# Optimization experiments

Measured on AMD Instinct MI355X. Metric: run time of the kernel, lower is better.

## Reference

```python
import jax, jax.numpy as jnp
import numpy as np

D = 128          # hidden_dim
R = 16           # num_relations
N = 50000        # num_nodes
E = 800000       # num_edges
P = 256          # number of candidate paths
L = 4            # path length in nodes (max_path_length=3 edges)
NUM_LAYERS = 2


def _layer_norm(x, g, b, eps=1e-5):
    mu = jnp.mean(x, axis=-1, keepdims=True)
    var = jnp.var(x, axis=-1, keepdims=True)
    return (x - mu) * jax.lax.rsqrt(var + eps) * g + b


def _lstm(x, W_ih, W_hh, b):
    # x: (P, L, 2D) -> final hidden state (P, D). PyTorch gate order i,f,g,o.
    h0 = jnp.zeros((x.shape[0], D), x.dtype)
    c0 = jnp.zeros((x.shape[0], D), x.dtype)
    xs = jnp.swapaxes(x, 0, 1)  # (L, P, 2D)

    def step(carry, xt):
        h, c = carry
        gates = xt @ W_ih.T + h @ W_hh.T + b
        i, f, g, o = jnp.split(gates, 4, axis=-1)
        c = jax.nn.sigmoid(f) * c + jax.nn.sigmoid(i) * jnp.tanh(g)
        h = jax.nn.sigmoid(o) * jnp.tanh(c)
        return (h, c), None

    (h, _), _ = jax.lax.scan(step, (h0, c0), xs)
    return h


def setup_inputs() -> dict:
    key = jax.random.key(0)
    ks = jax.random.split(key, 24)
    s = 0.02
    inp = {
        'node_features': jax.random.normal(ks[0], (N, D), jnp.float32),
        'edge_index': jax.random.randint(ks[1], (2, E), 0, N),
        'edge_types': jax.random.randint(ks[2], (E,), 0, R),
        'query_embedding': jax.random.normal(ks[3], (D,), jnp.float32),
        'path_nodes': jax.random.randint(ks[4], (P, L), 0, N),
        'path_relations': jax.random.randint(ks[5], (P, L - 1), 0, R),
        # RGCN params (stacked over layers)
        'W_self': jax.random.normal(ks[6], (NUM_LAYERS, D, D), jnp.float32) * s,
        'b_self': jnp.zeros((NUM_LAYERS, D), jnp.float32),
        'W_rel': jax.random.normal(ks[7], (NUM_LAYERS, R, D, D), jnp.float32) * s,
        'ln_g': jnp.ones((NUM_LAYERS, D), jnp.float32),
        'ln_b': jnp.zeros((NUM_LAYERS, D), jnp.float32),
        # PathEncoder
        'rel_emb': jax.random.normal(ks[8], (R, D), jnp.float32) * s,
        'W_ih_f': jax.random.normal(ks[9], (4 * D, 2 * D), jnp.float32) * s,
        'W_hh_f': jax.random.normal(ks[10], (4 * D, D), jnp.float32) * s,
        'b_f': jnp.zeros((4 * D,), jnp.float32),
        'W_ih_b': jax.random.normal(ks[11], (4 * D, 2 * D), jnp.float32) * s,
        'W_hh_b': jax.random.normal(ks[12], (4 * D, D), jnp.float32) * s,
        'b_b': jnp.zeros((4 * D,), jnp.float32),
        'W_op': jax.random.normal(ks[13], (D, 2 * D), jnp.float32) * s,
        'b_op': jnp.zeros((D,), jnp.float32),
        # similarity scorer
        'W_s1': jax.random.normal(ks[14], (D, 2 * D), jnp.float32) * s,
        'b_s1': jnp.zeros((D,), jnp.float32),
        'W_s2': jax.random.normal(ks[15], (1, D), jnp.float32) * s,
        'b_s2': jnp.zeros((1,), jnp.float32),
    }
    return inp


def reference(node_features, edge_index, edge_types, query_embedding,
              path_nodes, path_relations,
              W_self, b_self, W_rel, ln_g, ln_b,
              rel_emb, W_ih_f, W_hh_f, b_f, W_ih_b, W_hh_b, b_b, W_op, b_op,
              W_s1, b_s1, W_s2, b_s2):
    src, dst = edge_index[0], edge_index[1]
    n = node_features.shape[0]
    deg = jnp.zeros((n,), node_features.dtype).at[dst].add(1.0)
    denom = jnp.maximum(deg, 1.0)[:, None]

    # ---- encode_subgraph: RGCN layers + LayerNorm ----
    x = node_features
    for l in range(NUM_LAYERS):
        trans = jnp.einsum('nd,rdk->rnk', x, W_rel[l])       # (R, N, D)
        msg = trans[edge_types, src]                          # (E, D) gather
        agg = jax.ops.segment_sum(msg, dst, num_segments=n) / denom
        x = jax.nn.relu(x @ W_self[l] + b_self[l] + agg)
        x = _layer_norm(x, ln_g[l], ln_b[l])
    encoded = x

    # ---- PathEncoder, batched over P paths ----
    pn = encoded[path_nodes]                                  # (P, L, D)
    rf = rel_emb[path_relations]                              # (P, L-1, D)
    zero_rel = jnp.zeros((rf.shape[0], 1, D), rf.dtype)
    rf = jnp.concatenate([zero_rel, rf], axis=1)              # (P, L, D)
    seq = jnp.concatenate([pn, rf], axis=-1)                  # (P, L, 2D)

    h_f = _lstm(seq, W_ih_f, W_hh_f, b_f)                     # forward final h
    h_b = _lstm(seq[:, ::-1, :], W_ih_b, W_hh_b, b_b)         # backward final h
    pe = jnp.concatenate([h_f, h_b], axis=-1)                 # (P, 2D)
    pe = jax.nn.relu(pe @ W_op.T + b_op)                      # (P, D)

    # ---- similarity scorer ----
    q = jnp.broadcast_to(query_embedding[None, :], pe.shape)
    comb = jnp.concatenate([pe, q], axis=-1)                  # (P, 2D)
    hdn = jax.nn.relu(comb @ W_s1.T + b_s1)
    sim = jax.nn.sigmoid(hdn @ W_s2.T + b_s2).squeeze(-1)     # (P,)

    return encoded, pe, sim
```

## Files before the change

kernel.cpp:

```cpp
#include <hip/hip_runtime.h>


#define NN 50000
#define EE 800000
#define DD 128
#define RR 16
#define PP 256
#define PADN 50048
#define NSLOT 17
#define CSTRIDE 136

typedef __attribute__((ext_vector_type(4))) float f32x4;
typedef __attribute__((ext_vector_type(2))) float f32x2;
typedef __attribute__((ext_vector_type(8))) short s16x8;

__device__ __forceinline__ float bf2f(unsigned int u16v){
    unsigned int u = u16v << 16;
    return __builtin_bit_cast(float, u);
}
__device__ __forceinline__ unsigned short f2bf(float f){
    unsigned int u = __builtin_bit_cast(unsigned int, f);
    u = u + 0x7fffu + ((u >> 16) & 1u);
    return (unsigned short)(u >> 16);
}

__global__ void k_hist(const int* __restrict__ dst, int* __restrict__ deg,
                       int* __restrict__ rank){
    int e = blockIdx.x*256 + threadIdx.x;
    if (e < EE) rank[e] = atomicAdd(&deg[dst[e]], 1);
}
__global__ void k_scan1(const int* __restrict__ deg, int* __restrict__ bsum){
    __shared__ int sm[256];
    int t = threadIdx.x, i = blockIdx.x*256 + t;
    sm[t] = (i < NN) ? deg[i] : 0;
    __syncthreads();
    for (int o = 128; o > 0; o >>= 1){
        if (t < o) sm[t] += sm[t+o];
        __syncthreads();
    }
    if (t == 0) bsum[blockIdx.x] = sm[0];
}
__global__ void k_scan2(const int* __restrict__ bsum, int* __restrict__ boff){
    __shared__ int sm[256];
    int t = threadIdx.x;
    int v = (t < 196) ? bsum[t] : 0;
    sm[t] = v;
    __syncthreads();
    for (int o = 1; o < 256; o <<= 1){
        int x = (t >= o) ? sm[t-o] : 0;
        __syncthreads();
        sm[t] += x;
        __syncthreads();
    }
    boff[t] = sm[t] - v;
}
__global__ void k_scan3(const int* __restrict__ deg, const int* __restrict__ boff,
                        int* __restrict__ row_start){
    __shared__ int sm[256];
    int t = threadIdx.x, i = blockIdx.x*256 + t;
    int v = (i < NN) ? deg[i] : 0;
    sm[t] = v;
    __syncthreads();
    for (int o = 1; o < 256; o <<= 1){
        int x = (t >= o) ? sm[t-o] : 0;
        __syncthreads();
        sm[t] += x;
        __syncthreads();
    }
    if (i < NN) row_start[i] = boff[blockIdx.x] + sm[t] - v;
    if (i == 0) row_start[NN] = EE;
}

#define NB_FILL 3125
#define NB_CVT  25024
#define NB_PREP 3968
__global__ void k_fused(const int* __restrict__ src, const int* __restrict__ dst,
                        const int* __restrict__ et, const int* __restrict__ row_start,
                        const int* __restrict__ rank, unsigned int* __restrict__ csr,
                        const float* __restrict__ nf, unsigned short* __restrict__ xb,
                        const float* __restrict__ W_rel, const float* __restrict__ W_self,
                        const float* __restrict__ Wihf, const float* __restrict__ Wihb,
                        const float* __restrict__ Whhf, const float* __restrict__ Whhb,
                        const float* __restrict__ Wop,  const float* __restrict__ Ws1,
                        unsigned short* __restrict__ Bcat,
                        float* __restrict__ Wiht, float* __restrict__ Whht,
                        float* __restrict__ Wopt, float* __restrict__ Ws1t){
    int b = blockIdx.x;
    if (b < NB_FILL){
        int e = b*256 + threadIdx.x;
        int pos = row_start[dst[e]] + rank[e];
        csr[pos] = ((unsigned int)et[e] << 16) | (unsigned int)src[e];
        return;
    }
    if (b < NB_FILL + NB_CVT){
        int i = (b - NB_FILL)*256 + threadIdx.x;
        int r  = i >> 7;
        int dd = i & 127;
        int d  = (((dd >> 3) ^ (r & 15)) << 3) | (dd & 7);
        xb[i] = (r < NN) ? f2bf(nf[(size_t)r*DD + d]) : (unsigned short)0;
        return;
    }
    int i = (b - NB_FILL - NB_CVT)*256 + threadIdx.x;
    if (i < 557056){
        int l  = i / (NSLOT*DD*DD);
        int r  = i % (NSLOT*DD*DD);
        int s  = r / (DD*DD);
        int r2 = r % (DD*DD);
        int ko = r2 / DD;
        int dd = r2 % DD;
        int d  = (((dd >> 3) ^ (ko & 15)) << 3) | (dd & 7);
        float v = (s < RR) ? W_rel[(((size_t)(l*RR + s))*DD + d)*DD + ko]
                           : W_self[((size_t)l*DD + d)*DD + ko];
        Bcat[i] = f2bf(v);
        return;
    }
    int i2 = i - 557056;
    if (i2 < 131072){ int j=i2/512, g=i2%512; Wiht[i2] = Wihf[g*256+j]; }
    else if (i2 < 262144){ int i3=i2-131072; int j=i3/512, g=i3%512; Wiht[131072+i3] = Wihb[g*256+j]; }
    else if (i2 < 327680){ int i3=i2-262144; int j=i3/512, g=i3%512; Whht[i3] = Whhf[g*128+j]; }
    else if (i2 < 393216){ int i3=i2-327680; int j=i3/512, g=i3%512; Whht[65536+i3] = Whhb[g*128+j]; }
    else if (i2 < 425984){ int i3=i2-393216; int j=i3/128, k=i3%128; Wopt[i3] = Wop[k*256+j]; }
    else if (i2 < 458752){ int i3=i2-425984; int j=i3/128, k=i3%128; Ws1t[i3] = Ws1[k*256+j]; }
}

__global__ __launch_bounds__(256, 2) void k_gemm(const unsigned short* __restrict__ A,
                                                 const unsigned short* __restrict__ Bt,
                                                 unsigned short* __restrict__ C)
{
    __shared__ unsigned short S[32768];
    unsigned short* As = S;
    unsigned short* Bs = S + 16384;
    const int m0 = blockIdx.x * 128;
    const int s  = blockIdx.y;
    const int tid  = threadIdx.x;
    const int wave = tid >> 6;
    const int lane = tid & 63;

    const unsigned short* gA = A + ((size_t)m0 + wave*32)*DD + lane*8;
    const unsigned short* gB = Bt + ((size_t)s*DD + wave*32)*DD + lane*8;
    unsigned short* lA = As + (wave*32)*DD;
    unsigned short* lB = Bs + (wave*32)*DD;
    for (int i = 0; i < 8; ++i){
        __builtin_amdgcn_global_load_lds((__attribute__((address_space(1))) const void*)(gA + i*512),
                                         (__attribute__((address_space(3))) void*)(lA + i*512), 16, 0, 0);
        __builtin_amdgcn_global_load_lds((__attribute__((address_space(1))) const void*)(gB + i*512),
                                         (__attribute__((address_space(3))) void*)(lB + i*512), 16, 0, 0);
    }
    __syncthreads();

    const int wm = wave & 1, wn = wave >> 1;
    f32x4 acc[4][4];
    for (int a=0;a<4;++a) for (int b=0;b<4;++b) acc[a][b] = (f32x4){0.f,0.f,0.f,0.f};

    for (int kb = 0; kb < 4; ++kb){
        const int cx = (((kb << 2) + (lane >> 4)) ^ (lane & 15)) << 3;
        s16x8 af[4], bfr[4];
        for (int mi=0;mi<4;++mi)
            af[mi] = *(const s16x8*)(As + (wm*64 + mi*16 + (lane&15))*DD + cx);
        for (int ni=0;ni<4;++ni)
            bfr[ni] = *(const s16x8*)(Bs + (wn*64 + ni*16 + (lane&15))*DD + cx);
        for (int mi=0;mi<4;++mi)
            for (int ni=0;ni<4;++ni)
                acc[mi][ni] = __builtin_amdgcn_mfma_f32_16x16x32_bf16(af[mi], bfr[ni], acc[mi][ni], 0, 0, 0);
    }
    __syncthreads();
    unsigned short* Cs = S;
    for (int mi=0;mi<4;++mi){
        int mrow0 = wm*64 + mi*16 + ((lane>>4)<<2);
        for (int ni=0;ni<4;++ni){
            int coln = wn*64 + ni*16 + (lane&15);
            for (int r=0;r<4;++r)
                Cs[(mrow0+r)*CSTRIDE + coln] = f2bf(acc[mi][ni][r]);
        }
    }
    __syncthreads();
    for (int ps = 0; ps < 8; ++ps){
        int idx = ps*256 + tid;
        int row = idx >> 4, seg = idx & 15;
        int m = m0 + row;
        if (m < NN)
            *(s16x8*)(C + ((size_t)s*NN + m)*DD + seg*8) = *(const s16x8*)(Cs + row*CSTRIDE + seg*8);
    }
}

__global__ __launch_bounds__(256) void k_aggfin(
    const unsigned short* __restrict__ trans, const unsigned int* __restrict__ csr,
    const int* __restrict__ row_start,
    const float* __restrict__ bs, const float* __restrict__ lg, const float* __restrict__ lb,
    float* __restrict__ xf, unsigned short* __restrict__ xb, int write_f)
{
    int nd = blockIdx.x*4 + (threadIdx.x >> 6);
    int lane = threadIdx.x & 63;
    int half = lane >> 5;
    int sl   = lane & 31;
    if (nd >= NN){
        if (!write_f && nd < PADN) ((unsigned int*)xb)[(size_t)nd*64 + lane] = 0u;
        return;
    }
    int rs = row_start[nd], re = row_start[nd+1];
    float a0 = 0.f, a1 = 0.f, a2 = 0.f, a3 = 0.f;
    int e = rs + half;
    for (; e + 2 < re; e += 4){
        unsigned int v1 = csr[e], v2 = csr[e+2];
        unsigned long long p1 = *((const unsigned long long*)(trans +
            ((size_t)(v1 >> 16)*NN + (v1 & 0xffffu))*DD) + sl);
        unsigned long long p2 = *((const unsigned long long*)(trans +
            ((size_t)(v2 >> 16)*NN + (v2 & 0xffffu))*DD) + sl);
        unsigned int l1 = (unsigned int)p1, h1 = (unsigned int)(p1 >> 32);
        unsigned int l2 = (unsigned int)p2, h2 = (unsigned int)(p2 >> 32);
        a0 += bf2f(l1 & 0xffffu) + bf2f(l2 & 0xffffu);
        a1 += bf2f(l1 >> 16)     + bf2f(l2 >> 16);
        a2 += bf2f(h1 & 0xffffu) + bf2f(h2 & 0xffffu);
        a3 += bf2f(h1 >> 16)     + bf2f(h2 >> 16);
    }
    if (e < re){
        unsigned int v1 = csr[e];
        unsigned long long p1 = *((const unsigned long long*)(trans +
            ((size_t)(v1 >> 16)*NN + (v1 & 0xffffu))*DD) + sl);
        unsigned int l1 = (unsigned int)p1, h1 = (unsigned int)(p1 >> 32);
        a0 += bf2f(l1 & 0xffffu);
        a1 += bf2f(l1 >> 16);
        a2 += bf2f(h1 & 0xffffu);
        a3 += bf2f(h1 >> 16);
    }
    a0 += __shfl_xor(a0, 32);
    a1 += __shfl_xor(a1, 32);
    a2 += __shfl_xor(a2, 32);
    a3 += __shfl_xor(a3, 32);

    float invd = 1.f / fmaxf((float)(re - rs), 1.f);
    unsigned long long sv = *((const unsigned long long*)(trans +
        ((size_t)16*NN + nd)*DD) + sl);
    unsigned int slo = (unsigned int)sv, shi = (unsigned int)(sv >> 32);
    f32x4 bv = *(const f32x4*)&bs[sl*4];
    float y0 = bf2f(slo & 0xffffu) + bv[0] + a0*invd;
    float y1 = bf2f(slo >> 16)     + bv[1] + a1*invd;
    float y2 = bf2f(shi & 0xffffu) + bv[2] + a2*invd;
    float y3 = bf2f(shi >> 16)     + bv[3] + a3*invd;
    y0 = fmaxf(y0, 0.f); y1 = fmaxf(y1, 0.f);
    y2 = fmaxf(y2, 0.f); y3 = fmaxf(y3, 0.f);
    float s1 = y0 + y1 + y2 + y3;
    float s2 = y0*y0 + y1*y1 + y2*y2 + y3*y3;
    for (int off = 32; off > 0; off >>= 1){
        s1 += __shfl_xor(s1, off);
        s2 += __shfl_xor(s2, off);
    }
    float mu  = s1 * (1.f/256.f);
    float var = s2 * (1.f/256.f) - mu*mu;
    float inv = rsqrtf(var + 1e-5f);
    f32x4 gv = *(const f32x4*)&lg[sl*4];
    f32x4 lbv = *(const f32x4*)&lb[sl*4];
    float o0 = (y0 - mu)*inv*gv[0] + lbv[0];
    float o1 = (y1 - mu)*inv*gv[1] + lbv[1];
    float o2 = (y2 - mu)*inv*gv[2] + lbv[2];
    float o3 = (y3 - mu)*inv*gv[3] + lbv[3];
    if (half) return;
    if (write_f){
        *(f32x4*)(xf + (size_t)nd*DD + sl*4) = (f32x4){o0, o1, o2, o3};
    } else {
        unsigned int d0 = (unsigned int)f2bf(o0) | ((unsigned int)f2bf(o1) << 16);
        unsigned int d1 = (unsigned int)f2bf(o2) | ((unsigned int)f2bf(o3) << 16);
        int dw = (((sl >> 1) ^ (nd & 15)) << 2) + ((sl & 1) << 1);
        *((unsigned long long*)((unsigned int*)xb + (size_t)nd*64 + dw)) =
            (unsigned long long)d0 | ((unsigned long long)d1 << 32);
    }
}

__global__ __launch_bounds__(256) void k_gin(const float* __restrict__ enc,
                                             const int* __restrict__ pn,
                                             const int* __restrict__ pr,
                                             const float* __restrict__ rel_emb,
                                             const float* __restrict__ Wiht,
                                             float* __restrict__ gi){
    int b = blockIdx.x;
    int dir = b >> 7;
    int blk = b & 127;
    int pairs0 = blk * 8;
    int tid = threadIdx.x;
    int group = tid >> 7;
    int tl = tid & 127;
    __shared__ float sq[8][256];
    for (int k = 0; k < 2; ++k){
        int idx = tid + 256*k;
        int row = idx >> 6;
        int off = (idx & 63) * 4;
        int pair = pairs0 + row;
        int p = pair >> 2, tt = pair & 3;
        int tsel = dir ? (3 - tt) : tt;
        f32x4 v;
        if (off < 128){
            int node = pn[p*4 + tsel];
            v = *(const f32x4*)&enc[(size_t)node*DD + off];
        } else if (tsel == 0){
            v = (f32x4){0.f,0.f,0.f,0.f};
        } else {
            int rel = pr[p*3 + (tsel-1)];
            v = *(const f32x4*)&rel_emb[(size_t)rel*DD + (off-128)];
        }
        *(f32x4*)&sq[row][off] = v;
    }
    __syncthreads();
    const float* W = Wiht + (size_t)dir*131072;
    float acc[4][4];
    for (int a=0;a<4;++a) for (int g=0;g<4;++g) acc[a][g]=0.f;
    for (int j4 = 0; j4 < 256; j4 += 4){
        f32x4 sv[4];
        for (int q=0;q<4;++q) sv[q] = *(const f32x4*)&sq[group*4+q][j4];
        for (int jj = 0; jj < 4; ++jj){
            int j = j4 + jj;
            float w0 = W[(size_t)j*512 + tl];
            float w1 = W[(size_t)j*512 + tl + 128];
            float w2 = W[(size_t)j*512 + tl + 256];
            float w3 = W[(size_t)j*512 + tl + 384];
            for (int q=0;q<4;++q){
                float sval = sv[q][jj];
                acc[q][0] += sval*w0;
                acc[q][1] += sval*w1;
                acc[q][2] += sval*w2;
                acc[q][3] += sval*w3;
            }
        }
    }
    for (int q=0;q<4;++q){
        int pair = pairs0 + group*4 + q;
        float* dstp = gi + ((size_t)dir*1024 + pair)*512;
        dstp[tl]     = acc[q][0];
        dstp[tl+128] = acc[q][1];
        dstp[tl+256] = acc[q][2];
        dstp[tl+384] = acc[q][3];
    }
}
__global__ __launch_bounds__(256) void k_rec(const float* __restrict__ gi,
                                             const float* __restrict__ Whht,
                                             const float* __restrict__ b_f,
                                             const float* __restrict__ b_b,
                                             float* __restrict__ hbuf){
    int b = blockIdx.x;
    int dir = b >> 6;
    int pg = b & 63;
    int p0 = pg * 4;
    int tid = threadIdx.x;
    int group = tid >> 7;
    int tl = tid & 127;
    __shared__ float hs[4][128], cs[4][128], gb[4][512];
    {
        int it = tid;       hs[it>>7][it&127] = 0.f; cs[it>>7][it&127] = 0.f;
        it = tid + 256;     hs[it>>7][it&127] = 0.f; cs[it>>7][it&127] = 0.f;
    }
    __syncthreads();
    const float* W = Whht + (size_t)dir*65536;
    const float* bias = dir ? b_b : b_f;
    float bb0 = bias[tl], bb1 = bias[tl+128], bb2 = bias[tl+256], bb3 = bias[tl+384];
    for (int t = 0; t < 4; ++t){
        float acc[2][4];
        for (int pl = 0; pl < 2; ++pl){
            int p = p0 + group*2 + pl;
            const float* gp = gi + ((size_t)dir*1024 + p*4 + t)*512;
            acc[pl][0] = gp[tl]     + bb0;
            acc[pl][1] = gp[tl+128] + bb1;
            acc[pl][2] = gp[tl+256] + bb2;
            acc[pl][3] = gp[tl+384] + bb3;
        }
        for (int j4 = 0; j4 < 128; j4 += 4){
            f32x4 hv0 = *(const f32x4*)&hs[group*2][j4];
            f32x4 hv1 = *(const f32x4*)&hs[group*2+1][j4];
            for (int jj = 0; jj < 4; ++jj){
                int j = j4 + jj;
                float w0 = W[(size_t)j*512 + tl];
                float w1 = W[(size_t)j*512 + tl + 128];
                float w2 = W[(size_t)j*512 + tl + 256];
                float w3 = W[(size_t)j*512 + tl + 384];
                float h0 = hv0[jj], h1 = hv1[jj];
                acc[0][0] += h0*w0; acc[0][1] += h0*w1; acc[0][2] += h0*w2; acc[0][3] += h0*w3;
                acc[1][0] += h1*w0; acc[1][1] += h1*w1; acc[1][2] += h1*w2; acc[1][3] += h1*w3;
            }
        }
        for (int pl = 0; pl < 2; ++pl){
            int pidx = group*2 + pl;
            gb[pidx][tl]     = acc[pl][0];
            gb[pidx][tl+128] = acc[pl][1];
            gb[pidx][tl+256] = acc[pl][2];
            gb[pidx][tl+384] = acc[pl][3];
        }
        __syncthreads();
        for (int r = 0; r < 2; ++r){
            int it = tid + 256*r;
            int pidx = it >> 7, k = it & 127;
            float giv = gb[pidx][k], gfv = gb[pidx][128+k], ggv = gb[pidx][256+k], gov = gb[pidx][384+k];
            float si = 1.f/(1.f + expf(-giv));
            float sf = 1.f/(1.f + expf(-gfv));
            float so = 1.f/(1.f + expf(-gov));
            float cn = sf*cs[pidx][k] + si*tanhf(ggv);
            cs[pidx][k] = cn;
            hs[pidx][k] = so*tanhf(cn);
        }
        __syncthreads();
    }
    for (int r = 0; r < 2; ++r){
        int it = tid + 256*r;
        int pidx = it >> 7, k = it & 127;
        hbuf[((size_t)dir*PP + p0 + pidx)*DD + k] = hs[pidx][k];
    }
}
__global__ __launch_bounds__(256) void k_head(const float* __restrict__ hbuf,
    const float* __restrict__ query, const float* __restrict__ Wopt, const float* __restrict__ Ws1t,
    const float* __restrict__ b_op, const float* __restrict__ b_s1,
    const float* __restrict__ W_s2, const float* __restrict__ b_s2,
    float* __restrict__ out)
{
    int pb = blockIdx.x * 8;
    int tid = threadIdx.x;
    __shared__ float cat[8][256];
    __shared__ float pe_l[8][128];
    __shared__ float hd_l[8][128];
    __shared__ float qs[128];
    __shared__ float part[8][2];
    for (int k = 0; k < 8; ++k){
        int i = tid + 256*k;
        int p = i >> 8, j = i & 255;
        float v = (j < 128) ? hbuf[(size_t)(pb+p)*DD + j]
                            : hbuf[(size_t)(PP + pb + p)*DD + (j-128)];
        cat[p][j] = v;
    }
    if (tid < 128) qs[tid] = query[tid];
    __syncthreads();
    int k = tid & 127;
    int sub = tid >> 7;
    for (int r = 0; r < 4; ++r){
        int p = sub + 2*r;
        float a = b_op[k];
        for (int j = 0; j < 256; ++j) a += Wopt[j*128 + k] * cat[p][j];
        a = fmaxf(a, 0.f);
        pe_l[p][k] = a;
        out[(size_t)NN*DD + (size_t)(pb+p)*DD + k] = a;
    }
    __syncthreads();
    for (int r = 0; r < 4; ++r){
        int p = sub + 2*r;
        float a = b_s1[k];
        for (int j = 0; j < 128; ++j) a += Ws1t[j*128 + k] * pe_l[p][j];
        for (int j = 0; j < 128; ++j) a += Ws1t[(128+j)*128 + k] * qs[j];
        hd_l[p][k] = fmaxf(a, 0.f);
    }
    __syncthreads();
    for (int r = 0; r < 4; ++r){
        int p = sub + 2*r;
        float v = W_s2[k] * hd_l[p][k];
        for (int off = 32; off > 0; off >>= 1) v += __shfl_xor(v, off);
        if ((tid & 63) == 0) part[p][(tid>>6)&1] = v;
    }
    __syncthreads();
    if (tid < 8){
        float sv = part[tid][0] + part[tid][1] + b_s2[0];
        out[(size_t)NN*DD + (size_t)PP*DD + pb + tid] = 1.f/(1.f + expf(-sv));
    }
}

extern "C" void kernel_launch(void* const* d_in, const int* in_sizes, int n_in,
                              void* d_out, int out_size, void* d_ws, size_t ws_size,
                              hipStream_t stream)
{
    (void)in_sizes; (void)n_in; (void)out_size; (void)ws_size;
    const float* nf      = (const float*)d_in[0];
    const int*   ei      = (const int*)d_in[1];
    const int*   et      = (const int*)d_in[2];
    const float* query   = (const float*)d_in[3];
    const int*   pn      = (const int*)d_in[4];
    const int*   pr      = (const int*)d_in[5];
    const float* W_self  = (const float*)d_in[6];
    const float* b_self  = (const float*)d_in[7];
    const float* W_rel   = (const float*)d_in[8];
    const float* ln_g    = (const float*)d_in[9];
    const float* ln_b    = (const float*)d_in[10];
    const float* rel_emb = (const float*)d_in[11];
    const float* W_ih_f  = (const float*)d_in[12];
    const float* W_hh_f  = (const float*)d_in[13];
    const float* b_f     = (const float*)d_in[14];
    const float* W_ih_b  = (const float*)d_in[15];
    const float* W_hh_b  = (const float*)d_in[16];
    const float* b_b     = (const float*)d_in[17];
    const float* W_op    = (const float*)d_in[18];
    const float* b_op    = (const float*)d_in[19];
    const float* W_s1    = (const float*)d_in[20];
    const float* b_s1    = (const float*)d_in[21];
    const float* W_s2    = (const float*)d_in[22];
    const float* b_s2    = (const float*)d_in[23];
    float* out = (float*)d_out;

    char* wp = (char*)d_ws;
    size_t off = 0;
    auto alloc = [&](size_t bytes)->void*{
        void* p = wp + off;
        off += (bytes + 255) & ~(size_t)255;
        return p;
    };
    int* deg        = (int*)alloc((size_t)NN*4);
    int* row_start  = (int*)alloc((size_t)(NN+1)*4);
    int* rank       = (int*)alloc((size_t)EE*4);
    int* bsum       = (int*)alloc(256*4);
    int* boff       = (int*)alloc(256*4);
    unsigned int* csr = (unsigned int*)alloc((size_t)EE*4);
    unsigned short* x0b   = (unsigned short*)alloc((size_t)PADN*DD*2);
    unsigned short* x1b   = (unsigned short*)alloc((size_t)PADN*DD*2);
    unsigned short* Bcat  = (unsigned short*)alloc((size_t)2*NSLOT*DD*DD*2);
    float* Wiht = (float*)alloc((size_t)262144*4);
    float* Whht = (float*)alloc((size_t)131072*4);
    float* Wopt = (float*)alloc((size_t)32768*4);
    float* Ws1t = (float*)alloc((size_t)32768*4);
    float* gi   = (float*)alloc((size_t)2*1024*512*4);
    float* hbuf = (float*)alloc((size_t)2*PP*DD*4);
    unsigned short* trans = (unsigned short*)alloc((size_t)NSLOT*NN*DD*2);

    hipMemsetAsync(deg, 0, (size_t)NN*4, stream);
    k_hist<<<(EE+255)/256, 256, 0, stream>>>(ei + EE, deg, rank);
    k_scan1<<<196, 256, 0, stream>>>(deg, bsum);
    k_scan2<<<1, 256, 0, stream>>>(bsum, boff);
    k_scan3<<<196, 256, 0, stream>>>(deg, boff, row_start);
    k_fused<<<NB_FILL + NB_CVT + NB_PREP, 256, 0, stream>>>(
        ei, ei + EE, et, row_start, rank, csr, nf, x0b,
        W_rel, W_self, W_ih_f, W_ih_b, W_hh_f, W_hh_b, W_op, W_s1,
        Bcat, Wiht, Whht, Wopt, Ws1t);
    for (int l = 0; l < 2; ++l){
        const unsigned short* xin = l ? x1b : x0b;
        const unsigned short* Bl  = Bcat + (size_t)l*NSLOT*DD*DD;
        k_gemm<<<dim3(PADN/128, NSLOT), 256, 0, stream>>>(xin, Bl, trans);
        if (l == 0)
            k_aggfin<<<PADN/4, 256, 0, stream>>>(trans, csr, row_start,
                b_self, ln_g, ln_b, nullptr, x1b, 0);
        else
            k_aggfin<<<PADN/4, 256, 0, stream>>>(trans, csr, row_start,
                b_self + DD, ln_g + DD, ln_b + DD, out, nullptr, 1);
    }
    k_gin<<<256, 256, 0, stream>>>(out, pn, pr, rel_emb, Wiht, gi);
    k_rec<<<128, 256, 0, stream>>>(gi, Whht, b_f, b_b, hbuf);
    k_head<<<32, 256, 0, stream>>>(hbuf, query, Wopt, Ws1t, b_op, b_s1, W_s2, b_s2, out);
}
```

Baseline: 521.4 us.

## Loop over relation slots inside GEMM block, reusing a 64-row A tile

The GEMM grid changes from (row tile × slot) to row tiles only. Each block loads a 64-row A tile once and loops over all 17 weight slots, reloading the 128x128 B slice each iteration. Each wave now computes 16 rows × 128 columns. This cuts repeated A reads and makes blocks smaller, at the cost of serialised B loads with two barriers per slot and less parallelism per block.

Result: slower. 550.9 us (+5.7%).

```diff
diff --git a/kernel.cpp b/kernel.cpp
--- a/kernel.cpp
+++ b/kernel.cpp
@@ -127,59 +127,58 @@
                                                  const unsigned short* __restrict__ Bt,
                                                  unsigned short* __restrict__ C)
 {
-    __shared__ unsigned short S[32768];
-    unsigned short* As = S;
-    unsigned short* Bs = S + 16384;
-    const int m0 = blockIdx.x * 128;
-    const int s  = blockIdx.y;
+    __shared__ unsigned short As[64*128];
+    __shared__ unsigned short Bs[128*128];
+    __shared__ unsigned short Cs[64*CSTRIDE];
+    const int m0 = blockIdx.x * 64;
     const int tid  = threadIdx.x;
     const int wave = tid >> 6;
     const int lane = tid & 63;
 
-    const unsigned short* gA = A + ((size_t)m0 + wave*32)*DD + lane*8;
-    const unsigned short* gB = Bt + ((size_t)s*DD + wave*32)*DD + lane*8;
-    unsigned short* lA = As + (wave*32)*DD;
-    unsigned short* lB = Bs + (wave*32)*DD;
-    for (int i = 0; i < 8; ++i){
-        __builtin_amdgcn_global_load_lds((__attribute__((address_space(1))) const void*)(gA + i*512),
-                                         (__attribute__((address_space(3))) void*)(lA + i*512), 16, 0, 0);
-        __builtin_amdgcn_global_load_lds((__attribute__((address_space(1))) const void*)(gB + i*512),
-                                         (__attribute__((address_space(3))) void*)(lB + i*512), 16, 0, 0);
-    }
-    __syncthreads();
-
-    const int wm = wave & 1, wn = wave >> 1;
-    f32x4 acc[4][4];
-    for (int a=0;a<4;++a) for (int b=0;b<4;++b) acc[a][b] = (f32x4){0.f,0.f,0.f,0.f};
-
-    for (int kb = 0; kb < 4; ++kb){
-        const int cx = (((kb << 2) + (lane >> 4)) ^ (lane & 15)) << 3;
-        s16x8 af[4], bfr[4];
-        for (int mi=0;mi<4;++mi)
-            af[mi] = *(const s16x8*)(As + (wm*64 + mi*16 + (lane&15))*DD + cx);
-        for (int ni=0;ni<4;++ni)
-            bfr[ni] = *(const s16x8*)(Bs + (wn*64 + ni*16 + (lane&15))*DD + cx);
-        for (int mi=0;mi<4;++mi)
-            for (int ni=0;ni<4;++ni)
-                acc[mi][ni] = __builtin_amdgcn_mfma_f32_16x16x32_bf16(af[mi], bfr[ni], acc[mi][ni], 0, 0, 0);
-    }
-    __syncthreads();
-    unsigned short* Cs = S;
-    for (int mi=0;mi<4;++mi){
-        int mrow0 = wm*64 + mi*16 + ((lane>>4)<<2);
-        for (int ni=0;ni<4;++ni){
-            int coln = wn*64 + ni*16 + (lane&15);
-            for (int r=0;r<4;++r)
-                Cs[(mrow0+r)*CSTRIDE + coln] = f2bf(acc[mi][ni][r]);
-        }
-    }
-    __syncthreads();
-    for (int ps = 0; ps < 8; ++ps){
-        int idx = ps*256 + tid;
-        int row = idx >> 4, seg = idx & 15;
-        int m = m0 + row;
-        if (m < NN)
-            *(s16x8*)(C + ((size_t)s*NN + m)*DD + seg*8) = *(const s16x8*)(Cs + row*CSTRIDE + seg*8);
+    {
+        const unsigned short* gA = A + ((size_t)m0 + wave*16)*DD + lane*8;
+        unsigned short* lA = As + (wave*16)*DD;
+        for (int i = 0; i < 4; ++i)
+            __builtin_amdgcn_global_load_lds((__attribute__((address_space(1))) const void*)(gA + i*512),
+                                             (__attribute__((address_space(3))) void*)(lA + i*512), 16, 0, 0);
+    }
+
+    for (int s = 0; s < NSLOT; ++s){
+        __syncthreads();
+        {
+            const unsigned short* gB = Bt + ((size_t)s*DD + wave*32)*DD + lane*8;
+            unsigned short* lB = Bs + (wave*32)*DD;
+            for (int i = 0; i < 8; ++i)
+                __builtin_amdgcn_global_load_lds((__attribute__((address_space(1))) const void*)(gB + i*512),
+                                                 (__attribute__((address_space(3))) void*)(lB + i*512), 16, 0, 0);
+        }
+        __syncthreads();
+
+        f32x4 acc[8];
+        for (int t = 0; t < 8; ++t) acc[t] = (f32x4){0.f,0.f,0.f,0.f};
+        for (int kb = 0; kb < 4; ++kb){
+            const int cx = (((kb << 2) + (lane >> 4)) ^ (lane & 15)) << 3;
+            s16x8 af = *(const s16x8*)(As + (wave*16 + (lane&15))*DD + cx);
+            for (int nt = 0; nt < 8; ++nt){
+                s16x8 bf = *(const s16x8*)(Bs + (nt*16 + (lane&15))*DD + cx);
+                acc[nt] = __builtin_amdgcn_mfma_f32_16x16x32_bf16(af, bf, acc[nt], 0, 0, 0);
+            }
+        }
+        int mrow0 = wave*16 + ((lane>>4)<<2);
+        for (int nt = 0; nt < 8; ++nt){
+            int coln = nt*16 + (lane&15);
+            for (int r = 0; r < 4; ++r)
+                Cs[(mrow0+r)*CSTRIDE + coln] = f2bf(acc[nt][r]);
+        }
+        for (int i = 0; i < 4; ++i){
+            int u = i*64 + lane;
+            int row = wave*16 + (u >> 4);
+            int seg = u & 15;
+            int m = m0 + row;
+            if (m < NN)
+                *(s16x8*)(C + ((size_t)s*NN + m)*DD + seg*8) =
+                    *(const s16x8*)(Cs + row*CSTRIDE + seg*8);
+        }
     }
 }
 
@@ -523,7 +522,7 @@
     for (int l = 0; l < 2; ++l){
         const unsigned short* xin = l ? x1b : x0b;
         const unsigned short* Bl  = Bcat + (size_t)l*NSLOT*DD*DD;
-        k_gemm<<<dim3(PADN/128, NSLOT), 256, 0, stream>>>(xin, Bl, trans);
+        k_gemm<<<PADN/64, 256, 0, stream>>>(xin, Bl, trans);
         if (l == 0)
             k_aggfin<<<PADN/4, 256, 0, stream>>>(trans, csr, row_start,
                 b_self, ln_g, ln_b, nullptr, x1b, 0);
```
